# Kernel optimization log

Hardware: AMD Instinct MI355X
Metric: run time of the kernel (lower is better)

The kernel has to match this reference:

```python
import jax, jax.numpy as jnp
import numpy as np

QUERY_DIM = 512
KEY_DIM = 512
NUM_HEADS = 16
HEAD_DIM = QUERY_DIM // NUM_HEADS


def setup_inputs() -> dict:
    key = jax.random.key(0)
    ks = jax.random.split(key, 10)
    B, T, S = 4, 2048, 2048
    s_q = 1.0 / np.sqrt(QUERY_DIM)
    s_k = 1.0 / np.sqrt(KEY_DIM)
    return {
        "x": jax.random.normal(ks[0], (B, T, QUERY_DIM), dtype=jnp.float32),
        "context": jax.random.normal(ks[1], (B, S, KEY_DIM), dtype=jnp.float32),
        "Wq": jax.random.normal(ks[2], (QUERY_DIM, QUERY_DIM), dtype=jnp.float32) * s_q,
        "bq": jnp.zeros((QUERY_DIM,), dtype=jnp.float32),
        "Wk": jax.random.normal(ks[3], (KEY_DIM, QUERY_DIM), dtype=jnp.float32) * s_k,
        "bk": jnp.zeros((QUERY_DIM,), dtype=jnp.float32),
        "Wv": jax.random.normal(ks[4], (KEY_DIM, QUERY_DIM), dtype=jnp.float32) * s_k,
        "bv": jnp.zeros((QUERY_DIM,), dtype=jnp.float32),
        "Wo": jax.random.normal(ks[5], (QUERY_DIM, QUERY_DIM), dtype=jnp.float32) * s_q,
        "bo": jnp.zeros((QUERY_DIM,), dtype=jnp.float32),
    }


def reference(x, context, Wq, bq, Wk, bk, Wv, bv, Wo, bo):
    B, T, C = x.shape
    S = context.shape[1]
    H, D = NUM_HEADS, HEAD_DIM
    scale = D ** -0.5
    # projections -> [B, H, T/S, D]
    q = (x @ Wq + bq).reshape(B, T, H, D).transpose(0, 2, 1, 3)
    k = (context @ Wk + bk).reshape(B, S, H, D).transpose(0, 2, 1, 3)
    v = (context @ Wv + bv).reshape(B, S, H, D).transpose(0, 2, 1, 3)
    # explicit attention matrix [B, H, T, S] (faithful to the unfused original)
    attn = jnp.einsum("bhtd,bhsd->bhts", q, k) * scale
    attn = jax.nn.softmax(attn, axis=-1)  # dropout is identity in eval mode
    out = jnp.einsum("bhts,bhsd->bhtd", attn, v)
    out = out.transpose(0, 2, 1, 3).reshape(B, T, C)
    return out @ Wo + bo
```

## Files before the change

### kernel.cpp

```cpp
#include <hip/hip_runtime.h>
#include <hip/hip_bf16.h>
#include <cmath>

typedef __bf16 bf16;
typedef __bf16 bf16x2 __attribute__((ext_vector_type(2)));
typedef __bf16 bf16x4 __attribute__((ext_vector_type(4)));
typedef __bf16 bf16x8 __attribute__((ext_vector_type(8)));
typedef float floatx4 __attribute__((ext_vector_type(4)));
typedef unsigned int uintx2 __attribute__((ext_vector_type(2)));
typedef unsigned int uintx4 __attribute__((ext_vector_type(4)));

#define MFMA_BF16(a, b, c) __builtin_amdgcn_mfma_f32_16x16x32_bf16((a), (b), (c), 0, 0, 0)

#if defined(__has_builtin)
#if __has_builtin(__builtin_amdgcn_global_load_lds)
#define HAVE_GLL 1
#endif
#if __has_builtin(__builtin_amdgcn_cvt_pk_bf16_f32)
#define HAVE_PKCVT 1
#endif
#if __has_builtin(__builtin_amdgcn_permlane32_swap) && __has_builtin(__builtin_amdgcn_permlane16_swap)
#define HAVE_PLSWAP 1
#endif
#endif

__device__ __forceinline__ void stage16(const bf16* g, bf16* ldsbase, int lane) {
#ifdef HAVE_GLL
    __builtin_amdgcn_global_load_lds((const __attribute__((address_space(1))) unsigned int*)g,
                                     (__attribute__((address_space(3))) unsigned int*)ldsbase,
                                     16, 0, 0);
#else
    *(int4*)(ldsbase + lane * 8) = *(const int4*)g;
#endif
}

__device__ __forceinline__ unsigned pk2(float a, float b) {
    bf16x2 t;
#ifdef HAVE_PKCVT
    t = __builtin_amdgcn_cvt_pk_bf16_f32(a, b);
#else
    t[0] = (bf16)a;
    t[1] = (bf16)b;
#endif
    return __builtin_bit_cast(unsigned, t);
}

__device__ __forceinline__ uintx2 p32swap(unsigned x, unsigned y) {
#ifdef HAVE_PLSWAP
    auto r = __builtin_amdgcn_permlane32_swap(x, y, false, false);
    uintx2 o;
    o[0] = r[0];
    o[1] = r[1];
    return o;
#else
    const int lane = threadIdx.x & 63;
    const unsigned px = __shfl(x, lane ^ 32);
    const unsigned py = __shfl(y, lane ^ 32);
    uintx2 o;
    o[0] = (lane & 32) ? py : x;
    o[1] = (lane & 32) ? y : px;
    return o;
#endif
}

__device__ __forceinline__ uintx2 p16swap(unsigned x, unsigned y) {
#ifdef HAVE_PLSWAP
    auto r = __builtin_amdgcn_permlane16_swap(x, y, false, false);
    uintx2 o;
    o[0] = r[0];
    o[1] = r[1];
    return o;
#else
    const int lane = threadIdx.x & 63;
    const unsigned px = __shfl(x, lane ^ 16);
    const unsigned py = __shfl(y, lane ^ 16);
    uintx2 o;
    o[0] = (lane & 16) ? py : x;
    o[1] = (lane & 16) ? y : px;
    return o;
#endif
}

__device__ __forceinline__ int detect_bf16(const void* x) {
    const unsigned short* u = (const unsigned short*)x;
    const int lane = threadIdx.x & 63;
    const unsigned short w0 = u[4 * lane], w1 = u[4 * lane + 2];
    const int e0 = (w0 >> 7) & 0xFF, e1 = (w1 >> 7) & 0xFF;
    const unsigned long long b0 = __ballot(e0 >= 96 && e0 <= 158);
    const unsigned long long b1 = __ballot(e1 >= 96 && e1 <= 158);
    return (__popcll(b0) + __popcll(b1)) >= 90;
}

struct PrepArgs {
    const void* x;
    const void* ctx;
    const void* W[4];
    const void* bias[4];
    bf16* xc;
    bf16* ctxc;
    bf16* WT[4];
    bf16* biasc;
};

__global__ __launch_bounds__(256) void prep(PrepArgs a) {
    const int tid = threadIdx.x;
    const int f = detect_bf16(a.x);
    const int bid = blockIdx.x;
    if (bid < 1024) {
        const int w = bid >> 8, tileid = bid & 255;
        const int bx = tileid & 15, by = tileid >> 4;
        const void* __restrict__ in = a.W[w];
        bf16* __restrict__ out = a.WT[w];
        __shared__ bf16 tile[32][33];
        const int tx = tid & 31, ty = tid >> 5;
        const int x = bx * 32 + tx;
        const int y0 = by * 32;
#pragma unroll
        for (int yy = ty; yy < 32; yy += 8) {
            const size_t idx = (size_t)(y0 + yy) * 512 + x;
            const float v = f ? (float)((const bf16*)in)[idx] : ((const float*)in)[idx];
            tile[yy][tx] = (bf16)v;
        }
        __syncthreads();
        const int xo = by * 32 + tx;
        const int y1 = bx * 32;
#pragma unroll
        for (int yy = ty; yy < 32; yy += 8)
            out[(size_t)(y1 + yy) * 512 + xo] = tile[tx][yy];
    } else if (bid < 5120) {
        if (f) return;
        const int seg = (bid >= 3072);
        const void* src = seg ? a.ctx : a.x;
        bf16* dst = seg ? a.ctxc : a.xc;
        const int off = (bid - (seg ? 3072 : 1024)) * 256 + tid;
        const float4 p = ((const float4*)src)[2 * off];
        const float4 q = ((const float4*)src)[2 * off + 1];
        bf16x8 o;
        o[0] = (bf16)p.x; o[1] = (bf16)p.y; o[2] = (bf16)p.z; o[3] = (bf16)p.w;
        o[4] = (bf16)q.x; o[5] = (bf16)q.y; o[6] = (bf16)q.z; o[7] = (bf16)q.w;
        *(bf16x8*)(dst + (size_t)off * 8) = o;
    } else {
        for (int e = tid; e < 2048; e += 256) {
            const int seg = e >> 9, off = e & 511;
            const float v =
                f ? (float)((const bf16*)a.bias[seg])[off] : ((const float*)a.bias[seg])[off];
            a.biasc[seg * 512 + off] = (bf16)v;
        }
    }
}

struct QkvArgs {
    const void* xraw;
    const void* ctxraw;
    const bf16* Aconv[3];
    const bf16* Wt[3];
    const bf16* bias;
    bf16* out[3];
    float scale[3];
};

__global__ __launch_bounds__(256) void gemm_qkv(QkvArgs a) {
    __shared__ __align__(16) bf16 lA[2][128 * 32];
    __shared__ __align__(16) bf16 lB[2][128 * 32];
    const int z = blockIdx.z;
    const int f = detect_bf16(a.xraw);
    const bf16* __restrict__ A =
        f ? (const bf16*)(z == 0 ? a.xraw : a.ctxraw) : a.Aconv[z];
    const bf16* __restrict__ Wt = a.Wt[z];
    const int tid = threadIdx.x, wave = tid >> 6, lane = tid & 63;
    const int qd = lane >> 4, j = lane & 15;
    const int m0 = blockIdx.x * 128, n0 = blockIdx.y * 128;
    const int wrow = (wave & 1) * 64, wcol = (wave >> 1) * 64;
    const int srow = wave * 16 + (lane >> 2);
    const int scol = (lane & 3) * 8;
    const bf16* agp = A + (size_t)(m0 + srow) * 512 + scol;
    const bf16* bgp = Wt + (size_t)(n0 + srow) * 512 + scol;

    auto stage = [&](int buf, int k0) {
        stage16(agp + k0, &lA[buf][wave * 512], lane);
        stage16(agp + k0 + (size_t)64 * 512, &lA[buf][wave * 512 + 2048], lane);
        stage16(bgp + k0, &lB[buf][wave * 512], lane);
        stage16(bgp + k0 + (size_t)64 * 512, &lB[buf][wave * 512 + 2048], lane);
    };

    floatx4 acc[4][4] = {};

    stage(0, 0);
    int cur = 0;
#pragma unroll 1
    for (int it = 0; it < 16; ++it) {
        if (it < 15) {
            stage(cur ^ 1, (it + 1) * 32);
            asm volatile("s_waitcnt vmcnt(4)" ::: "memory");
        } else {
            asm volatile("s_waitcnt vmcnt(0)" ::: "memory");
        }
        __builtin_amdgcn_sched_barrier(0);
        __builtin_amdgcn_s_barrier();
        __builtin_amdgcn_sched_barrier(0);

        bf16x8 af[4], bfr[4];
#pragma unroll
        for (int i = 0; i < 4; ++i) {
            af[i] = *(const bf16x8*)(&lA[cur][(wrow + i * 16 + j) * 32 + qd * 8]);
            bfr[i] = *(const bf16x8*)(&lB[cur][(wcol + i * 16 + j) * 32 + qd * 8]);
        }
        if (z < 2) {
#pragma unroll
            for (int nt = 0; nt < 4; ++nt)
#pragma unroll
                for (int rf = 0; rf < 4; ++rf)
                    acc[nt][rf] = MFMA_BF16(bfr[nt], af[rf], acc[nt][rf]);
        } else {
#pragma unroll
            for (int rf = 0; rf < 4; ++rf)
#pragma unroll
                for (int nt = 0; nt < 4; ++nt)
                    acc[rf][nt] = MFMA_BF16(af[rf], bfr[nt], acc[rf][nt]);
        }

        __builtin_amdgcn_sched_barrier(0);
        __builtin_amdgcn_s_barrier();
        __builtin_amdgcn_sched_barrier(0);
        cur ^= 1;
    }

    const float scale = a.scale[z];
    const bf16* bias = a.bias + z * 512;
    bf16* __restrict__ C = a.out[z];
    if (z < 2) {
#pragma unroll
        for (int nt = 0; nt < 4; ++nt) {
            const int nb = n0 + wcol + nt * 16 + qd * 4;
            const bf16x4 bv4 = *(const bf16x4*)(bias + nb);
            const int h = nb >> 5, d0 = nb & 31;
#pragma unroll
            for (int rf = 0; rf < 4; ++rf) {
                const int m = m0 + wrow + rf * 16 + j;
                const int bb = m >> 11, t = m & 2047;
                bf16x4 pk;
#pragma unroll
                for (int r = 0; r < 4; ++r)
                    pk[r] = (bf16)((acc[nt][rf][r] + (float)bv4[r]) * scale);
                *(bf16x4*)(&C[(((size_t)bb * 16 + h) * 2048 + t) * 32 + d0]) = pk;
            }
        }
    } else {
#pragma unroll
        for (int nt = 0; nt < 4; ++nt) {
            const int n = n0 + wcol + nt * 16 + j;
            const float bv = (float)bias[n];
            const int h = n >> 5, d = n & 31;
#pragma unroll
            for (int rf = 0; rf < 4; ++rf) {
                const int t0 = m0 + wrow + rf * 16 + qd * 4;
                const int bb = t0 >> 11, s = t0 & 2047;
                bf16x4 pk;
#pragma unroll
                for (int r = 0; r < 4; ++r) pk[r] = (bf16)(acc[rf][nt][r] + bv);
                *(bf16x4*)(&C[(((size_t)bb * 16 + h) * 32 + d) * 2048 + s]) = pk;
            }
        }
    }
}

__device__ __forceinline__ void gll16kv(const bf16* g, bf16* lds) {
#ifdef HAVE_GLL
    __builtin_amdgcn_global_load_lds((const __attribute__((address_space(1))) unsigned int*)g,
                                     (__attribute__((address_space(3))) unsigned int*)lds,
                                     16, 0, 0);
#else
    *(int4*)(lds + (threadIdx.x & 63) * 8) = *(const int4*)g;
#endif
}

__global__ __launch_bounds__(256, 4) void attn_kernel(const bf16* __restrict__ Q,
                                                      const bf16* __restrict__ Kh,
                                                      const bf16* __restrict__ Vt,
                                                      bf16* __restrict__ O) {
    const int tid = threadIdx.x;
    const int wave = tid >> 6, lane = tid & 63;
    const int qd = lane >> 4, j = lane & 15;
    const int bh = blockIdx.x;
    const int b = bh >> 4, h = bh & 15;
    const int tw = blockIdx.y * 128 + wave * 32;

    __shared__ __align__(16) bf16 lsK[2][2][2048];
    __shared__ __align__(16) bf16 lsV[2][2][2048];

    const bf16* qbase = Q + ((size_t)bh * 2048 + tw) * 32;
    const bf16* kbase = Kh + (size_t)bh * 2048 * 32;
    const bf16* vbase = Vt + (size_t)bh * 32 * 2048;

    bf16x8 qf[2];
#pragma unroll
    for (int tf = 0; tf < 2; ++tf)
        qf[tf] = *(const bf16x8*)(qbase + (size_t)(tf * 16 + j) * 32 + qd * 8);

    const bf16* ksrc = kbase + (size_t)(wave * 16 + j) * 32 + qd * 8;
    const bf16* vsrc =
        vbase + (size_t)((wave >> 1) * 16 + j) * 2048 + (wave & 1) * 32 + qd * 8;
    bf16* kdst = &lsK[0][0][wave * 512];
    bf16* vdst = &lsV[0][0][wave * 512];

    auto stage = [&](int buf, int s0) {
        gll16kv(ksrc + (size_t)s0 * 32, kdst + buf * 4096);
        gll16kv(ksrc + (size_t)(s0 + 64) * 32, kdst + buf * 4096 + 2048);
        gll16kv(vsrc + s0, vdst + buf * 4096);
        gll16kv(vsrc + s0 + 64, vdst + buf * 4096 + 2048);
    };

    bf16x8 ones;
#pragma unroll
    for (int e = 0; e < 8; ++e) ones[e] = (bf16)1.0f;

    const floatx4 zero = {0.f, 0.f, 0.f, 0.f};
    floatx4 oacc[2][2] = {};
    floatx4 dacc[2] = {};

    auto qk = [&](const bf16* lk, bf16x8* pf) {
        bf16x8 kf[4];
#pragma unroll
        for (int sf = 0; sf < 4; ++sf)
            kf[sf] = *(const bf16x8*)(lk + sf * 512 + lane * 8);
#pragma unroll
        for (int tf = 0; tf < 2; ++tf) {
            floatx4 sc[4];
#pragma unroll
            for (int sf = 0; sf < 4; ++sf) sc[sf] = MFMA_BF16(kf[sf], qf[tf], zero);
            unsigned SW[4][2];
#pragma unroll
            for (int sf = 0; sf < 4; ++sf) {
                const float e0 = __builtin_amdgcn_exp2f(sc[sf][0]);
                const float e1 = __builtin_amdgcn_exp2f(sc[sf][1]);
                const float e2 = __builtin_amdgcn_exp2f(sc[sf][2]);
                const float e3 = __builtin_amdgcn_exp2f(sc[sf][3]);
                SW[sf][0] = pk2(e0, e1);
                SW[sf][1] = pk2(e2, e3);
            }
            const uintx2 a0 = p32swap(SW[0][0], SW[1][0]);
            const uintx2 a1 = p32swap(SW[0][1], SW[1][1]);
            const uintx2 c0 = p32swap(SW[2][0], SW[3][0]);
            const uintx2 c1 = p32swap(SW[2][1], SW[3][1]);
            const uintx2 t0 = p16swap(a0[0], a0[1]);
            const uintx2 t1 = p16swap(a1[0], a1[1]);
            const uintx2 t2 = p16swap(c0[0], c0[1]);
            const uintx2 t3 = p16swap(c1[0], c1[1]);
            uintx4 w0, w1;
            w0[0] = t0[0]; w0[1] = t1[0]; w0[2] = t0[1]; w0[3] = t1[1];
            w1[0] = t2[0]; w1[1] = t3[0]; w1[2] = t2[1]; w1[3] = t3[1];
            pf[tf * 2 + 0] = __builtin_bit_cast(bf16x8, w0);
            pf[tf * 2 + 1] = __builtin_bit_cast(bf16x8, w1);
        }
    };
    auto pv = [&](const bf16* lv, const bf16x8* pf) {
        bf16x8 vf[4];
#pragma unroll
        for (int i = 0; i < 4; ++i)
            vf[i] = *(const bf16x8*)(lv + i * 512 + lane * 8);
#pragma unroll
        for (int tf = 0; tf < 2; ++tf) {
            oacc[tf][0] = MFMA_BF16(pf[tf * 2 + 0], vf[0], oacc[tf][0]);
            oacc[tf][1] = MFMA_BF16(pf[tf * 2 + 0], vf[2], oacc[tf][1]);
            dacc[tf] = MFMA_BF16(pf[tf * 2 + 0], ones, dacc[tf]);
            oacc[tf][0] = MFMA_BF16(pf[tf * 2 + 1], vf[1], oacc[tf][0]);
            oacc[tf][1] = MFMA_BF16(pf[tf * 2 + 1], vf[3], oacc[tf][1]);
            dacc[tf] = MFMA_BF16(pf[tf * 2 + 1], ones, dacc[tf]);
        }
    };

    stage(0, 0);

    int cur = 0;
#pragma unroll 1
    for (int ph = 0; ph < 16; ++ph) {
        if (ph < 15) {
            stage(cur ^ 1, (ph + 1) * 128);
            asm volatile("s_waitcnt vmcnt(4)" ::: "memory");
        } else {
            asm volatile("s_waitcnt vmcnt(0)" ::: "memory");
        }
        __builtin_amdgcn_sched_barrier(0);
        __builtin_amdgcn_s_barrier();
        __builtin_amdgcn_sched_barrier(0);

        bf16x8 pfA[4], pfB[4];
        qk(&lsK[cur][0][0], pfA);
        qk(&lsK[cur][1][0], pfB);
        pv(&lsV[cur][0][0], pfA);
        pv(&lsV[cur][1][0], pfB);

        __builtin_amdgcn_sched_barrier(0);
        __builtin_amdgcn_s_barrier();
        __builtin_amdgcn_sched_barrier(0);
        cur ^= 1;
    }

#pragma unroll
    for (int tf = 0; tf < 2; ++tf)
#pragma unroll
        for (int r = 0; r < 4; ++r) {
            const float inv = 1.0f / dacc[tf][r];
            const int t = tw + tf * 16 + qd * 4 + r;
#pragma unroll
            for (int dt = 0; dt < 2; ++dt)
                O[((size_t)b * 2048 + t) * 512 + h * 32 + dt * 16 + j] =
                    (bf16)(oacc[tf][dt][r] * inv);
        }
}

__global__ __launch_bounds__(256) void gemm_out(const bf16* __restrict__ A,
                                                const bf16* __restrict__ Wt,
                                                const bf16* __restrict__ bias,
                                                void* __restrict__ C,
                                                const void* __restrict__ xraw) {
    __shared__ __align__(16) bf16 lA[2][128 * 32];
    __shared__ __align__(16) bf16 lB[2][128 * 32];
    const int oflag = detect_bf16(xraw);
    const int tid = threadIdx.x, wave = tid >> 6, lane = tid & 63;
    const int qd = lane >> 4, j = lane & 15;
    const int m0 = blockIdx.x * 128, n0 = blockIdx.y * 128;
    const int wrow = (wave & 1) * 64, wcol = (wave >> 1) * 64;
    const int srow = wave * 16 + (lane >> 2);
    const int scol = (lane & 3) * 8;
    const bf16* agp = A + (size_t)(m0 + srow) * 512 + scol;
    const bf16* bgp = Wt + (size_t)(n0 + srow) * 512 + scol;

    auto stage = [&](int buf, int k0) {
        stage16(agp + k0, &lA[buf][wave * 512], lane);
        stage16(agp + k0 + (size_t)64 * 512, &lA[buf][wave * 512 + 2048], lane);
        stage16(bgp + k0, &lB[buf][wave * 512], lane);
        stage16(bgp + k0 + (size_t)64 * 512, &lB[buf][wave * 512 + 2048], lane);
    };

    floatx4 acc[4][4] = {};

    stage(0, 0);
    int cur = 0;
#pragma unroll 1
    for (int it = 0; it < 16; ++it) {
        if (it < 15) {
            stage(cur ^ 1, (it + 1) * 32);
            asm volatile("s_waitcnt vmcnt(4)" ::: "memory");
        } else {
            asm volatile("s_waitcnt vmcnt(0)" ::: "memory");
        }
        __builtin_amdgcn_sched_barrier(0);
        __builtin_amdgcn_s_barrier();
        __builtin_amdgcn_sched_barrier(0);

        bf16x8 af[4], bfr[4];
#pragma unroll
        for (int i = 0; i < 4; ++i) {
            af[i] = *(const bf16x8*)(&lA[cur][(wrow + i * 16 + j) * 32 + qd * 8]);
            bfr[i] = *(const bf16x8*)(&lB[cur][(wcol + i * 16 + j) * 32 + qd * 8]);
        }
#pragma unroll
        for (int nt = 0; nt < 4; ++nt)
#pragma unroll
            for (int rf = 0; rf < 4; ++rf)
                acc[nt][rf] = MFMA_BF16(bfr[nt], af[rf], acc[nt][rf]);

        __builtin_amdgcn_sched_barrier(0);
        __builtin_amdgcn_s_barrier();
        __builtin_amdgcn_sched_barrier(0);
        cur ^= 1;
    }

#pragma unroll
    for (int nt = 0; nt < 4; ++nt) {
        const int nb = n0 + wcol + nt * 16 + qd * 4;
        const bf16x4 bv4 = *(const bf16x4*)(bias + nb);
#pragma unroll
        for (int rf = 0; rf < 4; ++rf) {
            const int m = m0 + wrow + rf * 16 + j;
            if (oflag) {
                bf16x4 pk;
#pragma unroll
                for (int r = 0; r < 4; ++r) pk[r] = (bf16)(acc[nt][rf][r] + (float)bv4[r]);
                *(bf16x4*)((bf16*)C + (size_t)m * 512 + nb) = pk;
            } else {
                float4 v;
                v.x = acc[nt][rf][0] + (float)bv4[0];
                v.y = acc[nt][rf][1] + (float)bv4[1];
                v.z = acc[nt][rf][2] + (float)bv4[2];
                v.w = acc[nt][rf][3] + (float)bv4[3];
                *(float4*)((float*)C + (size_t)m * 512 + nb) = v;
            }
        }
    }
}

extern "C" void kernel_launch(void* const* d_in, const int* in_sizes, int n_in, void* d_out,
                              int out_size, void* d_ws, size_t ws_size, hipStream_t stream) {
    char* ws = (char*)d_ws;
    bf16* wqT = (bf16*)(ws + 1048576);
    bf16* wkT = (bf16*)(ws + 1572864);
    bf16* wvT = (bf16*)(ws + 2097152);
    bf16* woT = (bf16*)(ws + 2621440);
    bf16* biasc = (bf16*)(ws + 3145728);
    bf16* xc = (bf16*)(ws + 4194304);
    bf16* ctxc = (bf16*)(ws + 12582912);
    bf16* qws = (bf16*)(ws + 20971520);
    bf16* kws = (bf16*)(ws + 29360128);
    bf16* vtws = (bf16*)(ws + 37748736);
    bf16* aws = xc;

    PrepArgs pa;
    pa.x = d_in[0]; pa.ctx = d_in[1];
    pa.W[0] = d_in[2]; pa.W[1] = d_in[4]; pa.W[2] = d_in[6]; pa.W[3] = d_in[8];
    pa.bias[0] = d_in[3]; pa.bias[1] = d_in[5]; pa.bias[2] = d_in[7]; pa.bias[3] = d_in[9];
    pa.xc = xc; pa.ctxc = ctxc;
    pa.WT[0] = wqT; pa.WT[1] = wkT; pa.WT[2] = wvT; pa.WT[3] = woT;
    pa.biasc = biasc;
    prep<<<5121, 256, 0, stream>>>(pa);

    QkvArgs qa;
    qa.xraw = d_in[0]; qa.ctxraw = d_in[1];
    qa.Aconv[0] = xc; qa.Aconv[1] = ctxc; qa.Aconv[2] = ctxc;
    qa.Wt[0] = wqT; qa.Wt[1] = wkT; qa.Wt[2] = wvT;
    qa.bias = biasc;
    qa.out[0] = qws; qa.out[1] = kws; qa.out[2] = vtws;
    qa.scale[0] = 0.2550348593f; qa.scale[1] = 1.0f; qa.scale[2] = 1.0f;
    gemm_qkv<<<dim3(64, 4, 3), 256, 0, stream>>>(qa);

    attn_kernel<<<dim3(64, 16), 256, 0, stream>>>(qws, kws, vtws, aws);

    gemm_out<<<dim3(64, 4), 256, 0, stream>>>(aws, woT, biasc + 3 * 512, d_out, d_in[0]);
}
```

Measured before the change: 197.6 us.

## Fuse fp32-to-bf16 conversion and weight transpose into GEMM loaders, drop prep kernel

Removes the separate prep kernel that converted x/context to bf16 and transposed and converted the weights. The QKV and output GEMMs now load raw fp32 (or bf16) activations and weights into registers, pack them to bf16, and write them into LDS with an in-register transpose for W. This saves one launch and a full round trip of converted x/context through global memory. In exchange, the GEMM main loops lose the async global-to-LDS path, wait for all loads each iteration, and do scalar 2-byte LDS stores for the B tile, which may cause bank conflicts.

After: 210.6 us. 6.6% more time.

```diff
diff --git a/kernel.cpp b/kernel.cpp
--- a/kernel.cpp
+++ b/kernel.cpp
@@ -7,6 +7,7 @@
 typedef __bf16 bf16x4 __attribute__((ext_vector_type(4)));
 typedef __bf16 bf16x8 __attribute__((ext_vector_type(8)));
 typedef float floatx4 __attribute__((ext_vector_type(4)));
+typedef int intx4 __attribute__((ext_vector_type(4)));
 typedef unsigned int uintx2 __attribute__((ext_vector_type(2)));
 typedef unsigned int uintx4 __attribute__((ext_vector_type(4)));
 
@@ -34,6 +35,22 @@
 #endif
 }
 
+__device__ __forceinline__ float4 gload16f(const float* p) {
+    float4 r;
+    asm volatile("global_load_dwordx4 %0, %1, off" : "=v"(r) : "v"(p));
+    return r;
+}
+__device__ __forceinline__ bf16x8 gload16h(const bf16* p) {
+    intx4 r;
+    asm volatile("global_load_dwordx4 %0, %1, off" : "=v"(r) : "v"(p));
+    return __builtin_bit_cast(bf16x8, r);
+}
+#define VMCNT0()                                         \
+    do {                                                 \
+        asm volatile("s_waitcnt vmcnt(0)" ::: "memory"); \
+        __builtin_amdgcn_sched_barrier(0);               \
+    } while (0)
+
 __device__ __forceinline__ unsigned pk2(float a, float b) {
     bf16x2 t;
 #ifdef HAVE_PKCVT
@@ -43,6 +60,15 @@
     t[1] = (bf16)b;
 #endif
     return __builtin_bit_cast(unsigned, t);
+}
+
+__device__ __forceinline__ bf16x8 pack8(const float4& a, const float4& b) {
+    uintx4 w;
+    w[0] = pk2(a.x, a.y);
+    w[1] = pk2(a.z, a.w);
+    w[2] = pk2(b.x, b.y);
+    w[3] = pk2(b.z, b.w);
+    return __builtin_bit_cast(bf16x8, w);
 }
 
 __device__ __forceinline__ uintx2 p32swap(unsigned x, unsigned y) {
@@ -62,7 +88,6 @@
     return o;
 #endif
 }
-
 __device__ __forceinline__ uintx2 p16swap(unsigned x, unsigned y) {
 #ifdef HAVE_PLSWAP
     auto r = __builtin_amdgcn_permlane16_swap(x, y, false, false);
@@ -91,119 +116,97 @@
     return (__popcll(b0) + __popcll(b1)) >= 90;
 }
 
-struct PrepArgs {
-    const void* x;
-    const void* ctx;
-    const void* W[4];
-    const void* bias[4];
-    bf16* xc;
-    bf16* ctxc;
-    bf16* WT[4];
-    bf16* biasc;
-};
-
-__global__ __launch_bounds__(256) void prep(PrepArgs a) {
-    const int tid = threadIdx.x;
-    const int f = detect_bf16(a.x);
-    const int bid = blockIdx.x;
-    if (bid < 1024) {
-        const int w = bid >> 8, tileid = bid & 255;
-        const int bx = tileid & 15, by = tileid >> 4;
-        const void* __restrict__ in = a.W[w];
-        bf16* __restrict__ out = a.WT[w];
-        __shared__ bf16 tile[32][33];
-        const int tx = tid & 31, ty = tid >> 5;
-        const int x = bx * 32 + tx;
-        const int y0 = by * 32;
-#pragma unroll
-        for (int yy = ty; yy < 32; yy += 8) {
-            const size_t idx = (size_t)(y0 + yy) * 512 + x;
-            const float v = f ? (float)((const bf16*)in)[idx] : ((const float*)in)[idx];
-            tile[yy][tx] = (bf16)v;
-        }
-        __syncthreads();
-        const int xo = by * 32 + tx;
-        const int y1 = bx * 32;
-#pragma unroll
-        for (int yy = ty; yy < 32; yy += 8)
-            out[(size_t)(y1 + yy) * 512 + xo] = tile[tx][yy];
-    } else if (bid < 5120) {
-        if (f) return;
-        const int seg = (bid >= 3072);
-        const void* src = seg ? a.ctx : a.x;
-        bf16* dst = seg ? a.ctxc : a.xc;
-        const int off = (bid - (seg ? 3072 : 1024)) * 256 + tid;
-        const float4 p = ((const float4*)src)[2 * off];
-        const float4 q = ((const float4*)src)[2 * off + 1];
-        bf16x8 o;
-        o[0] = (bf16)p.x; o[1] = (bf16)p.y; o[2] = (bf16)p.z; o[3] = (bf16)p.w;
-        o[4] = (bf16)q.x; o[5] = (bf16)q.y; o[6] = (bf16)q.z; o[7] = (bf16)q.w;
-        *(bf16x8*)(dst + (size_t)off * 8) = o;
-    } else {
-        for (int e = tid; e < 2048; e += 256) {
-            const int seg = e >> 9, off = e & 511;
-            const float v =
-                f ? (float)((const bf16*)a.bias[seg])[off] : ((const float*)a.bias[seg])[off];
-            a.biasc[seg * 512 + off] = (bf16)v;
-        }
-    }
-}
-
 struct QkvArgs {
     const void* xraw;
     const void* ctxraw;
-    const bf16* Aconv[3];
-    const bf16* Wt[3];
-    const bf16* bias;
+    const void* W[3];
+    const void* bias[3];
     bf16* out[3];
     float scale[3];
 };
 
 __global__ __launch_bounds__(256) void gemm_qkv(QkvArgs a) {
-    __shared__ __align__(16) bf16 lA[2][128 * 32];
-    __shared__ __align__(16) bf16 lB[2][128 * 32];
+    __shared__ __align__(16) bf16 lsA[2][4096];
+    __shared__ __align__(16) bf16 lsB[2][4096];
     const int z = blockIdx.z;
     const int f = detect_bf16(a.xraw);
-    const bf16* __restrict__ A =
-        f ? (const bf16*)(z == 0 ? a.xraw : a.ctxraw) : a.Aconv[z];
-    const bf16* __restrict__ Wt = a.Wt[z];
     const int tid = threadIdx.x, wave = tid >> 6, lane = tid & 63;
     const int qd = lane >> 4, j = lane & 15;
     const int m0 = blockIdx.x * 128, n0 = blockIdx.y * 128;
     const int wrow = (wave & 1) * 64, wcol = (wave >> 1) * 64;
-    const int srow = wave * 16 + (lane >> 2);
-    const int scol = (lane & 3) * 8;
-    const bf16* agp = A + (size_t)(m0 + srow) * 512 + scol;
-    const bf16* bgp = Wt + (size_t)(n0 + srow) * 512 + scol;
+
+    const void* Araw = (z == 0) ? a.xraw : a.ctxraw;
+    const void* Wraw = a.W[z];
+
+    const int srow = wave * 16 + (lane >> 2), scol = (lane & 3) * 8;
+    const bf16* agp = (const bf16*)Araw + (size_t)(m0 + srow) * 512 + scol;
+    const float* Af = (const float*)Araw;
+    const int am = m0 + wave * 32 + (lane >> 1), ah = (lane & 1) * 16;
+    const int bk = lane >> 1, bnl = (lane & 1) * 8;
+    const bf16* Wh = (const bf16*)Wraw;
+    const float* Wf = (const float*)Wraw;
+    const size_t bcol = (size_t)(n0 + wave * 32 + bnl);
+
+    float4 ar[4], br[4];
+    bf16x8 bh0, bh1;
 
     auto stage = [&](int buf, int k0) {
-        stage16(agp + k0, &lA[buf][wave * 512], lane);
-        stage16(agp + k0 + (size_t)64 * 512, &lA[buf][wave * 512 + 2048], lane);
-        stage16(bgp + k0, &lB[buf][wave * 512], lane);
-        stage16(bgp + k0 + (size_t)64 * 512, &lB[buf][wave * 512 + 2048], lane);
+        if (f) {
+            stage16(agp + k0, &lsA[buf][wave * 512], lane);
+            stage16(agp + k0 + (size_t)64 * 512, &lsA[buf][wave * 512 + 2048], lane);
+            const bf16* bp = Wh + (size_t)(k0 + bk) * 512 + bcol;
+            bh0 = gload16h(bp);
+            bh1 = gload16h(bp + 16);
+        } else {
+            const float* ap = Af + (size_t)am * 512 + k0 + ah;
+            ar[0] = gload16f(ap);
+            ar[1] = gload16f(ap + 4);
+            ar[2] = gload16f(ap + 8);
+            ar[3] = gload16f(ap + 12);
+            const float* bp = Wf + (size_t)(k0 + bk) * 512 + bcol;
+            br[0] = gload16f(bp);
+            br[1] = gload16f(bp + 4);
+            br[2] = gload16f(bp + 16);
+            br[3] = gload16f(bp + 20);
+        }
+    };
+    auto finish = [&](int buf) {
+        bf16x8 b0, b1;
+        if (f) {
+            b0 = bh0;
+            b1 = bh1;
+        } else {
+            b0 = pack8(br[0], br[1]);
+            b1 = pack8(br[2], br[3]);
+            bf16* ad = &lsA[buf][(wave * 32 + (lane >> 1)) * 32 + ah];
+            *(bf16x8*)ad = pack8(ar[0], ar[1]);
+            *(bf16x8*)(ad + 8) = pack8(ar[2], ar[3]);
+        }
+        const int nb0 = wave * 32 + bnl;
+#pragma unroll
+        for (int e = 0; e < 8; ++e) {
+            lsB[buf][(nb0 + e) * 32 + bk] = b0[e];
+            lsB[buf][(nb0 + 16 + e) * 32 + bk] = b1[e];
+        }
     };
 
     floatx4 acc[4][4] = {};
 
     stage(0, 0);
+    VMCNT0();
+    finish(0);
+    __syncthreads();
+
     int cur = 0;
 #pragma unroll 1
     for (int it = 0; it < 16; ++it) {
-        if (it < 15) {
-            stage(cur ^ 1, (it + 1) * 32);
-            asm volatile("s_waitcnt vmcnt(4)" ::: "memory");
-        } else {
-            asm volatile("s_waitcnt vmcnt(0)" ::: "memory");
-        }
-        __builtin_amdgcn_sched_barrier(0);
-        __builtin_amdgcn_s_barrier();
-        __builtin_amdgcn_sched_barrier(0);
+        if (it < 15) stage(cur ^ 1, (it + 1) * 32);
 
         bf16x8 af[4], bfr[4];
 #pragma unroll
         for (int i = 0; i < 4; ++i) {
-            af[i] = *(const bf16x8*)(&lA[cur][(wrow + i * 16 + j) * 32 + qd * 8]);
-            bfr[i] = *(const bf16x8*)(&lB[cur][(wcol + i * 16 + j) * 32 + qd * 8]);
+            af[i] = *(const bf16x8*)(&lsA[cur][(wrow + i * 16 + j) * 32 + qd * 8]);
+            bfr[i] = *(const bf16x8*)(&lsB[cur][(wcol + i * 16 + j) * 32 + qd * 8]);
         }
         if (z < 2) {
 #pragma unroll
@@ -219,46 +222,56 @@
                     acc[rf][nt] = MFMA_BF16(af[rf], bfr[nt], acc[rf][nt]);
         }
 
-        __builtin_amdgcn_sched_barrier(0);
-        __builtin_amdgcn_s_barrier();
-        __builtin_amdgcn_sched_barrier(0);
+        if (it < 15) {
+            VMCNT0();
+            finish(cur ^ 1);
+        }
+        __syncthreads();
         cur ^= 1;
     }
 
     const float scale = a.scale[z];
-    const bf16* bias = a.bias + z * 512;
     bf16* __restrict__ C = a.out[z];
     if (z < 2) {
 #pragma unroll
         for (int nt = 0; nt < 4; ++nt) {
             const int nb = n0 + wcol + nt * 16 + qd * 4;
-            const bf16x4 bv4 = *(const bf16x4*)(bias + nb);
+            float bvf[4];
+            if (f) {
+                const bf16x4 t = *(const bf16x4*)((const bf16*)a.bias[z] + nb);
+#pragma unroll
+                for (int r = 0; r < 4; ++r) bvf[r] = (float)t[r];
+            } else {
+                const float4 t = *(const float4*)((const float*)a.bias[z] + nb);
+                bvf[0] = t.x; bvf[1] = t.y; bvf[2] = t.z; bvf[3] = t.w;
+            }
             const int h = nb >> 5, d0 = nb & 31;
 #pragma unroll
             for (int rf = 0; rf < 4; ++rf) {
                 const int m = m0 + wrow + rf * 16 + j;
-                const int bb = m >> 11, t = m & 2047;
+                const int bb2 = m >> 11, t = m & 2047;
                 bf16x4 pk;
 #pragma unroll
                 for (int r = 0; r < 4; ++r)
-                    pk[r] = (bf16)((acc[nt][rf][r] + (float)bv4[r]) * scale);
-                *(bf16x4*)(&C[(((size_t)bb * 16 + h) * 2048 + t) * 32 + d0]) = pk;
+                    pk[r] = (bf16)((acc[nt][rf][r] + bvf[r]) * scale);
+                *(bf16x4*)(&C[(((size_t)bb2 * 16 + h) * 2048 + t) * 32 + d0]) = pk;
             }
         }
     } else {
 #pragma unroll
         for (int nt = 0; nt < 4; ++nt) {
             const int n = n0 + wcol + nt * 16 + j;
-            const float bv = (float)bias[n];
+            const float bv = f ? (float)((const bf16*)a.bias[z])[n]
+                               : ((const float*)a.bias[z])[n];
             const int h = n >> 5, d = n & 31;
 #pragma unroll
             for (int rf = 0; rf < 4; ++rf) {
                 const int t0 = m0 + wrow + rf * 16 + qd * 4;
-                const int bb = t0 >> 11, s = t0 & 2047;
+                const int bb2 = t0 >> 11, s = t0 & 2047;
                 bf16x4 pk;
 #pragma unroll
                 for (int r = 0; r < 4; ++r) pk[r] = (bf16)(acc[rf][nt][r] + bv);
-                *(bf16x4*)(&C[(((size_t)bb * 16 + h) * 32 + d) * 2048 + s]) = pk;
+                *(bf16x4*)(&C[(((size_t)bb2 * 16 + h) * 32 + d) * 2048 + s]) = pk;
             }
         }
     }
@@ -410,50 +423,76 @@
 }
 
 __global__ __launch_bounds__(256) void gemm_out(const bf16* __restrict__ A,
-                                                const bf16* __restrict__ Wt,
-                                                const bf16* __restrict__ bias,
+                                                const void* __restrict__ Wraw,
+                                                const void* __restrict__ biasraw,
                                                 void* __restrict__ C,
                                                 const void* __restrict__ xraw) {
-    __shared__ __align__(16) bf16 lA[2][128 * 32];
-    __shared__ __align__(16) bf16 lB[2][128 * 32];
-    const int oflag = detect_bf16(xraw);
+    __shared__ __align__(16) bf16 lsA[2][4096];
+    __shared__ __align__(16) bf16 lsB[2][4096];
+    const int f = detect_bf16(xraw);
     const int tid = threadIdx.x, wave = tid >> 6, lane = tid & 63;
     const int qd = lane >> 4, j = lane & 15;
     const int m0 = blockIdx.x * 128, n0 = blockIdx.y * 128;
     const int wrow = (wave & 1) * 64, wcol = (wave >> 1) * 64;
-    const int srow = wave * 16 + (lane >> 2);
-    const int scol = (lane & 3) * 8;
+    const int srow = wave * 16 + (lane >> 2), scol = (lane & 3) * 8;
     const bf16* agp = A + (size_t)(m0 + srow) * 512 + scol;
-    const bf16* bgp = Wt + (size_t)(n0 + srow) * 512 + scol;
+    const int bk = lane >> 1, bnl = (lane & 1) * 8;
+    const bf16* Wh = (const bf16*)Wraw;
+    const float* Wf = (const float*)Wraw;
+    const size_t bcol = (size_t)(n0 + wave * 32 + bnl);
+
+    float4 br[4];
+    bf16x8 bh0, bh1;
 
     auto stage = [&](int buf, int k0) {
-        stage16(agp + k0, &lA[buf][wave * 512], lane);
-        stage16(agp + k0 + (size_t)64 * 512, &lA[buf][wave * 512 + 2048], lane);
-        stage16(bgp + k0, &lB[buf][wave * 512], lane);
-        stage16(bgp + k0 + (size_t)64 * 512, &lB[buf][wave * 512 + 2048], lane);
+        stage16(agp + k0, &lsA[buf][wave * 512], lane);
+        stage16(agp + k0 + (size_t)64 * 512, &lsA[buf][wave * 512 + 2048], lane);
+        if (f) {
+            const bf16* bp = Wh + (size_t)(k0 + bk) * 512 + bcol;
+            bh0 = gload16h(bp);
+            bh1 = gload16h(bp + 16);
+        } else {
+            const float* bp = Wf + (size_t)(k0 + bk) * 512 + bcol;
+            br[0] = gload16f(bp);
+            br[1] = gload16f(bp + 4);
+            br[2] = gload16f(bp + 16);
+            br[3] = gload16f(bp + 20);
+        }
+    };
+    auto finish = [&](int buf) {
+        bf16x8 b0, b1;
+        if (f) {
+            b0 = bh0;
+            b1 = bh1;
+        } else {
+            b0 = pack8(br[0], br[1]);
+            b1 = pack8(br[2], br[3]);
+        }
+        const int nb0 = wave * 32 + bnl;
+#pragma unroll
+        for (int e = 0; e < 8; ++e) {
+            lsB[buf][(nb0 + e) * 32 + bk] = b0[e];
+            lsB[buf][(nb0 + 16 + e) * 32 + bk] = b1[e];
+        }
     };
 
     floatx4 acc[4][4] = {};
 
     stage(0, 0);
+    VMCNT0();
+    finish(0);
+    __syncthreads();
+
     int cur = 0;
 #pragma unroll 1
     for (int it = 0; it < 16; ++it) {
-        if (it < 15) {
-            stage(cur ^ 1, (it + 1) * 32);
-            asm volatile("s_waitcnt vmcnt(4)" ::: "memory");
-        } else {
-            asm volatile("s_waitcnt vmcnt(0)" ::: "memory");
-        }
-        __builtin_amdgcn_sched_barrier(0);
-        __builtin_amdgcn_s_barrier();
-        __builtin_amdgcn_sched_barrier(0);
+        if (it < 15) stage(cur ^ 1, (it + 1) * 32);
 
         bf16x8 af[4], bfr[4];
 #pragma unroll
         for (int i = 0; i < 4; ++i) {
-            af[i] = *(const bf16x8*)(&lA[cur][(wrow + i * 16 + j) * 32 + qd * 8]);
-            bfr[i] = *(const bf16x8*)(&lB[cur][(wcol + i * 16 + j) * 32 + qd * 8]);
+            af[i] = *(const bf16x8*)(&lsA[cur][(wrow + i * 16 + j) * 32 + qd * 8]);
+            bfr[i] = *(const bf16x8*)(&lsB[cur][(wcol + i * 16 + j) * 32 + qd * 8]);
         }
 #pragma unroll
         for (int nt = 0; nt < 4; ++nt)
@@ -461,30 +500,40 @@
             for (int rf = 0; rf < 4; ++rf)
                 acc[nt][rf] = MFMA_BF16(bfr[nt], af[rf], acc[nt][rf]);
 
-        __builtin_amdgcn_sched_barrier(0);
-        __builtin_amdgcn_s_barrier();
-        __builtin_amdgcn_sched_barrier(0);
+        if (it < 15) {
+            VMCNT0();
+            finish(cur ^ 1);
+        }
+        __syncthreads();
         cur ^= 1;
     }
 
 #pragma unroll
     for (int nt = 0; nt < 4; ++nt) {
         const int nb = n0 + wcol + nt * 16 + qd * 4;
-        const bf16x4 bv4 = *(const bf16x4*)(bias + nb);
+        float bvf[4];
+        if (f) {
+            const bf16x4 t = *(const bf16x4*)((const bf16*)biasraw + nb);
+#pragma unroll
+            for (int r = 0; r < 4; ++r) bvf[r] = (float)t[r];
+        } else {
+            const float4 t = *(const float4*)((const float*)biasraw + nb);
+            bvf[0] = t.x; bvf[1] = t.y; bvf[2] = t.z; bvf[3] = t.w;
+        }
 #pragma unroll
         for (int rf = 0; rf < 4; ++rf) {
             const int m = m0 + wrow + rf * 16 + j;
-            if (oflag) {
+            if (f) {
                 bf16x4 pk;
 #pragma unroll
-                for (int r = 0; r < 4; ++r) pk[r] = (bf16)(acc[nt][rf][r] + (float)bv4[r]);
+                for (int r = 0; r < 4; ++r) pk[r] = (bf16)(acc[nt][rf][r] + bvf[r]);
                 *(bf16x4*)((bf16*)C + (size_t)m * 512 + nb) = pk;
             } else {
                 float4 v;
-                v.x = acc[nt][rf][0] + (float)bv4[0];
-                v.y = acc[nt][rf][1] + (float)bv4[1];
-                v.z = acc[nt][rf][2] + (float)bv4[2];
-                v.w = acc[nt][rf][3] + (float)bv4[3];
+                v.x = acc[nt][rf][0] + bvf[0];
+                v.y = acc[nt][rf][1] + bvf[1];
+                v.z = acc[nt][rf][2] + bvf[2];
+                v.w = acc[nt][rf][3] + bvf[3];
                 *(float4*)((float*)C + (size_t)m * 512 + nb) = v;
             }
         }
@@ -494,37 +543,20 @@
 extern "C" void kernel_launch(void* const* d_in, const int* in_sizes, int n_in, void* d_out,
                               int out_size, void* d_ws, size_t ws_size, hipStream_t stream) {
     char* ws = (char*)d_ws;
-    bf16* wqT = (bf16*)(ws + 1048576);
-    bf16* wkT = (bf16*)(ws + 1572864);
-    bf16* wvT = (bf16*)(ws + 2097152);
-    bf16* woT = (bf16*)(ws + 2621440);
-    bf16* biasc = (bf16*)(ws + 3145728);
-    bf16* xc = (bf16*)(ws + 4194304);
-    bf16* ctxc = (bf16*)(ws + 12582912);
+    bf16* aws = (bf16*)(ws + 4194304);
     bf16* qws = (bf16*)(ws + 20971520);
     bf16* kws = (bf16*)(ws + 29360128);
     bf16* vtws = (bf16*)(ws + 37748736);
-    bf16* aws = xc;
-
-    PrepArgs pa;
-    pa.x = d_in[0]; pa.ctx = d_in[1];
-    pa.W[0] = d_in[2]; pa.W[1] = d_in[4]; pa.W[2] = d_in[6]; pa.W[3] = d_in[8];
-    pa.bias[0] = d_in[3]; pa.bias[1] = d_in[5]; pa.bias[2] = d_in[7]; pa.bias[3] = d_in[9];
-    pa.xc = xc; pa.ctxc = ctxc;
-    pa.WT[0] = wqT; pa.WT[1] = wkT; pa.WT[2] = wvT; pa.WT[3] = woT;
-    pa.biasc = biasc;
-    prep<<<5121, 256, 0, stream>>>(pa);
 
     QkvArgs qa;
     qa.xraw = d_in[0]; qa.ctxraw = d_in[1];
-    qa.Aconv[0] = xc; qa.Aconv[1] = ctxc; qa.Aconv[2] = ctxc;
-    qa.Wt[0] = wqT; qa.Wt[1] = wkT; qa.Wt[2] = wvT;
-    qa.bias = biasc;
+    qa.W[0] = d_in[2]; qa.W[1] = d_in[4]; qa.W[2] = d_in[6];
+    qa.bias[0] = d_in[3]; qa.bias[1] = d_in[5]; qa.bias[2] = d_in[7];
     qa.out[0] = qws; qa.out[1] = kws; qa.out[2] = vtws;
     qa.scale[0] = 0.2550348593f; qa.scale[1] = 1.0f; qa.scale[2] = 1.0f;
     gemm_qkv<<<dim3(64, 4, 3), 256, 0, stream>>>(qa);
 
     attn_kernel<<<dim3(64, 16), 256, 0, stream>>>(qws, kws, vtws, aws);
 
-    gemm_out<<<dim3(64, 4), 256, 0, stream>>>(aws, woT, biasc + 3 * 512, d_out, d_in[0]);
-}
+    gemm_out<<<dim3(64, 4), 256, 0, stream>>>(aws, d_in[8], d_in[9], d_out, d_in[0]);
+}
```

## Fuse fp32-to-bf16 activation conversion into QKV GEMM A-operand staging

Applied to the files above, without the earlier changes.

Drops the separate conversion of x and context to bf16 from the prep kernel. The QKV GEMM now loads fp32 activations straight into registers, packs them to bf16, and writes them to a padded LDS tile while the next B tile streams in asynchronously. Biases are read raw in the epilogues instead of from a pre-converted buffer. This removes a full-activation write and re-read pass to global memory, but each QKV GEMM block now reads fp32 A (double the bytes), and K and V blocks each convert the context separately, in a loop that waits on all loads before every LDS write.

Measured after the change: 195.1 us. No clear change (-1.2%).

```diff
diff --git a/kernel.cpp b/kernel.cpp
--- a/kernel.cpp
+++ b/kernel.cpp
@@ -7,6 +7,7 @@
 typedef __bf16 bf16x4 __attribute__((ext_vector_type(4)));
 typedef __bf16 bf16x8 __attribute__((ext_vector_type(8)));
 typedef float floatx4 __attribute__((ext_vector_type(4)));
+typedef int intx4 __attribute__((ext_vector_type(4)));
 typedef unsigned int uintx2 __attribute__((ext_vector_type(2)));
 typedef unsigned int uintx4 __attribute__((ext_vector_type(4)));
 
@@ -34,6 +35,17 @@
 #endif
 }
 
+__device__ __forceinline__ float4 gload16f(const float* p) {
+    float4 r;
+    asm volatile("global_load_dwordx4 %0, %1, off" : "=v"(r) : "v"(p));
+    return r;
+}
+#define VMCNT0()                                         \
+    do {                                                 \
+        asm volatile("s_waitcnt vmcnt(0)" ::: "memory"); \
+        __builtin_amdgcn_sched_barrier(0);               \
+    } while (0)
+
 __device__ __forceinline__ unsigned pk2(float a, float b) {
     bf16x2 t;
 #ifdef HAVE_PKCVT
@@ -43,6 +55,15 @@
     t[1] = (bf16)b;
 #endif
     return __builtin_bit_cast(unsigned, t);
+}
+
+__device__ __forceinline__ bf16x8 pack8(const float4& a, const float4& b) {
+    uintx4 w;
+    w[0] = pk2(a.x, a.y);
+    w[1] = pk2(a.z, a.w);
+    w[2] = pk2(b.x, b.y);
+    w[3] = pk2(b.z, b.w);
+    return __builtin_bit_cast(bf16x8, w);
 }
 
 __device__ __forceinline__ uintx2 p32swap(unsigned x, unsigned y) {
@@ -62,7 +83,6 @@
     return o;
 #endif
 }
-
 __device__ __forceinline__ uintx2 p16swap(unsigned x, unsigned y) {
 #ifdef HAVE_PLSWAP
     auto r = __builtin_amdgcn_permlane16_swap(x, y, false, false);
@@ -91,119 +111,99 @@
     return (__popcll(b0) + __popcll(b1)) >= 90;
 }
 
-struct PrepArgs {
+struct PrepWArgs {
     const void* x;
-    const void* ctx;
     const void* W[4];
-    const void* bias[4];
-    bf16* xc;
-    bf16* ctxc;
     bf16* WT[4];
-    bf16* biasc;
 };
 
-__global__ __launch_bounds__(256) void prep(PrepArgs a) {
+__global__ __launch_bounds__(256) void prep_w(PrepWArgs a) {
     const int tid = threadIdx.x;
     const int f = detect_bf16(a.x);
     const int bid = blockIdx.x;
-    if (bid < 1024) {
-        const int w = bid >> 8, tileid = bid & 255;
-        const int bx = tileid & 15, by = tileid >> 4;
-        const void* __restrict__ in = a.W[w];
-        bf16* __restrict__ out = a.WT[w];
-        __shared__ bf16 tile[32][33];
-        const int tx = tid & 31, ty = tid >> 5;
-        const int x = bx * 32 + tx;
-        const int y0 = by * 32;
-#pragma unroll
-        for (int yy = ty; yy < 32; yy += 8) {
-            const size_t idx = (size_t)(y0 + yy) * 512 + x;
-            const float v = f ? (float)((const bf16*)in)[idx] : ((const float*)in)[idx];
-            tile[yy][tx] = (bf16)v;
-        }
-        __syncthreads();
-        const int xo = by * 32 + tx;
-        const int y1 = bx * 32;
-#pragma unroll
-        for (int yy = ty; yy < 32; yy += 8)
-            out[(size_t)(y1 + yy) * 512 + xo] = tile[tx][yy];
-    } else if (bid < 5120) {
-        if (f) return;
-        const int seg = (bid >= 3072);
-        const void* src = seg ? a.ctx : a.x;
-        bf16* dst = seg ? a.ctxc : a.xc;
-        const int off = (bid - (seg ? 3072 : 1024)) * 256 + tid;
-        const float4 p = ((const float4*)src)[2 * off];
-        const float4 q = ((const float4*)src)[2 * off + 1];
-        bf16x8 o;
-        o[0] = (bf16)p.x; o[1] = (bf16)p.y; o[2] = (bf16)p.z; o[3] = (bf16)p.w;
-        o[4] = (bf16)q.x; o[5] = (bf16)q.y; o[6] = (bf16)q.z; o[7] = (bf16)q.w;
-        *(bf16x8*)(dst + (size_t)off * 8) = o;
-    } else {
-        for (int e = tid; e < 2048; e += 256) {
-            const int seg = e >> 9, off = e & 511;
-            const float v =
-                f ? (float)((const bf16*)a.bias[seg])[off] : ((const float*)a.bias[seg])[off];
-            a.biasc[seg * 512 + off] = (bf16)v;
-        }
+    const int w = bid >> 8, tileid = bid & 255;
+    const int bx = tileid & 15, by = tileid >> 4;
+    const void* __restrict__ in = a.W[w];
+    bf16* __restrict__ out = a.WT[w];
+    __shared__ bf16 tile[32][33];
+    const int tx = tid & 31, ty = tid >> 5;
+    const int x = bx * 32 + tx;
+    const int y0 = by * 32;
+#pragma unroll
+    for (int yy = ty; yy < 32; yy += 8) {
+        const size_t idx = (size_t)(y0 + yy) * 512 + x;
+        const float v = f ? (float)((const bf16*)in)[idx] : ((const float*)in)[idx];
+        tile[yy][tx] = (bf16)v;
     }
+    __syncthreads();
+    const int xo = by * 32 + tx;
+    const int y1 = bx * 32;
+#pragma unroll
+    for (int yy = ty; yy < 32; yy += 8)
+        out[(size_t)(y1 + yy) * 512 + xo] = tile[tx][yy];
 }
 
 struct QkvArgs {
     const void* xraw;
     const void* ctxraw;
-    const bf16* Aconv[3];
     const bf16* Wt[3];
-    const bf16* bias;
+    const void* bias[3];
     bf16* out[3];
     float scale[3];
 };
 
 __global__ __launch_bounds__(256) void gemm_qkv(QkvArgs a) {
-    __shared__ __align__(16) bf16 lA[2][128 * 32];
-    __shared__ __align__(16) bf16 lB[2][128 * 32];
+    __shared__ __align__(16) bf16 lsA[2][128 * 40];
+    __shared__ __align__(16) bf16 lsB[2][4096];
     const int z = blockIdx.z;
     const int f = detect_bf16(a.xraw);
-    const bf16* __restrict__ A =
-        f ? (const bf16*)(z == 0 ? a.xraw : a.ctxraw) : a.Aconv[z];
-    const bf16* __restrict__ Wt = a.Wt[z];
     const int tid = threadIdx.x, wave = tid >> 6, lane = tid & 63;
     const int qd = lane >> 4, j = lane & 15;
     const int m0 = blockIdx.x * 128, n0 = blockIdx.y * 128;
     const int wrow = (wave & 1) * 64, wcol = (wave >> 1) * 64;
-    const int srow = wave * 16 + (lane >> 2);
-    const int scol = (lane & 3) * 8;
-    const bf16* agp = A + (size_t)(m0 + srow) * 512 + scol;
+
+    const void* Araw = (z == 0) ? a.xraw : a.ctxraw;
+    const bf16* __restrict__ Wt = a.Wt[z];
+
+    const int srow = wave * 16 + (lane >> 2), scol = (lane & 3) * 8;
+    const bf16* agp = (const bf16*)Araw + (size_t)(m0 + srow) * 512 + scol;
     const bf16* bgp = Wt + (size_t)(n0 + srow) * 512 + scol;
-
-    auto stage = [&](int buf, int k0) {
-        stage16(agp + k0, &lA[buf][wave * 512], lane);
-        stage16(agp + k0 + (size_t)64 * 512, &lA[buf][wave * 512 + 2048], lane);
-        stage16(bgp + k0, &lB[buf][wave * 512], lane);
-        stage16(bgp + k0 + (size_t)64 * 512, &lB[buf][wave * 512 + 2048], lane);
+    const float* Af = (const float*)Araw;
+    const int arow = wave * 32 + (lane >> 1);
+    const int ah = (lane & 1) * 16;
+
+    const int SA = f ? 32 : 40;
+
+    float4 ar[4];
+    auto stageB = [&](int buf, int k0) {
+        stage16(bgp + k0, &lsB[buf][wave * 512], lane);
+        stage16(bgp + k0 + (size_t)64 * 512, &lsB[buf][wave * 512 + 2048], lane);
+    };
+    auto loadA = [&](int k0) {
+        const float* ap = Af + (size_t)(m0 + arow) * 512 + k0 + ah;
+        ar[0] = gload16f(ap);
+        ar[1] = gload16f(ap + 4);
+        ar[2] = gload16f(ap + 8);
+        ar[3] = gload16f(ap + 12);
+    };
+    auto writeA = [&](int buf) {
+        bf16* ad = &lsA[buf][arow * 40 + ah];
+        *(bf16x8*)ad = pack8(ar[0], ar[1]);
+        *(bf16x8*)(ad + 8) = pack8(ar[2], ar[3]);
+    };
+    auto stageA1 = [&](int buf, int k0) {
+        stage16(agp + k0, &lsA[buf][wave * 512], lane);
+        stage16(agp + k0 + (size_t)64 * 512, &lsA[buf][wave * 512 + 2048], lane);
     };
 
     floatx4 acc[4][4] = {};
 
-    stage(0, 0);
-    int cur = 0;
-#pragma unroll 1
-    for (int it = 0; it < 16; ++it) {
-        if (it < 15) {
-            stage(cur ^ 1, (it + 1) * 32);
-            asm volatile("s_waitcnt vmcnt(4)" ::: "memory");
-        } else {
-            asm volatile("s_waitcnt vmcnt(0)" ::: "memory");
-        }
-        __builtin_amdgcn_sched_barrier(0);
-        __builtin_amdgcn_s_barrier();
-        __builtin_amdgcn_sched_barrier(0);
-
+    auto compute = [&](int cur) {
         bf16x8 af[4], bfr[4];
 #pragma unroll
         for (int i = 0; i < 4; ++i) {
-            af[i] = *(const bf16x8*)(&lA[cur][(wrow + i * 16 + j) * 32 + qd * 8]);
-            bfr[i] = *(const bf16x8*)(&lB[cur][(wcol + i * 16 + j) * 32 + qd * 8]);
+            af[i] = *(const bf16x8*)(&lsA[cur][(wrow + i * 16 + j) * SA + qd * 8]);
+            bfr[i] = *(const bf16x8*)(&lsB[cur][(wcol + i * 16 + j) * 32 + qd * 8]);
         }
         if (z < 2) {
 #pragma unroll
@@ -218,47 +218,95 @@
                 for (int nt = 0; nt < 4; ++nt)
                     acc[rf][nt] = MFMA_BF16(af[rf], bfr[nt], acc[rf][nt]);
         }
-
-        __builtin_amdgcn_sched_barrier(0);
-        __builtin_amdgcn_s_barrier();
-        __builtin_amdgcn_sched_barrier(0);
-        cur ^= 1;
+    };
+
+    if (f) {
+        stageA1(0, 0);
+        stageB(0, 0);
+        int cur = 0;
+#pragma unroll 1
+        for (int it = 0; it < 16; ++it) {
+            if (it < 15) {
+                stageA1(cur ^ 1, (it + 1) * 32);
+                stageB(cur ^ 1, (it + 1) * 32);
+                asm volatile("s_waitcnt vmcnt(4)" ::: "memory");
+            } else {
+                asm volatile("s_waitcnt vmcnt(0)" ::: "memory");
+            }
+            __builtin_amdgcn_sched_barrier(0);
+            __builtin_amdgcn_s_barrier();
+            __builtin_amdgcn_sched_barrier(0);
+            compute(cur);
+            __builtin_amdgcn_sched_barrier(0);
+            __builtin_amdgcn_s_barrier();
+            __builtin_amdgcn_sched_barrier(0);
+            cur ^= 1;
+        }
+    } else {
+        stageB(0, 0);
+        loadA(0);
+        VMCNT0();
+        writeA(0);
+        __syncthreads();
+        int cur = 0;
+#pragma unroll 1
+        for (int it = 0; it < 16; ++it) {
+            if (it < 15) {
+                stageB(cur ^ 1, (it + 1) * 32);
+                loadA((it + 1) * 32);
+            }
+            compute(cur);
+            if (it < 15) {
+                VMCNT0();
+                writeA(cur ^ 1);
+            }
+            __syncthreads();
+            cur ^= 1;
+        }
     }
 
     const float scale = a.scale[z];
-    const bf16* bias = a.bias + z * 512;
     bf16* __restrict__ C = a.out[z];
     if (z < 2) {
 #pragma unroll
         for (int nt = 0; nt < 4; ++nt) {
             const int nb = n0 + wcol + nt * 16 + qd * 4;
-            const bf16x4 bv4 = *(const bf16x4*)(bias + nb);
+            float bvf[4];
+            if (f) {
+                const bf16x4 t = *(const bf16x4*)((const bf16*)a.bias[z] + nb);
+#pragma unroll
+                for (int r = 0; r < 4; ++r) bvf[r] = (float)t[r];
+            } else {
+                const float4 t = *(const float4*)((const float*)a.bias[z] + nb);
+                bvf[0] = t.x; bvf[1] = t.y; bvf[2] = t.z; bvf[3] = t.w;
+            }
             const int h = nb >> 5, d0 = nb & 31;
 #pragma unroll
             for (int rf = 0; rf < 4; ++rf) {
                 const int m = m0 + wrow + rf * 16 + j;
-                const int bb = m >> 11, t = m & 2047;
+                const int bb2 = m >> 11, t = m & 2047;
                 bf16x4 pk;
 #pragma unroll
                 for (int r = 0; r < 4; ++r)
-                    pk[r] = (bf16)((acc[nt][rf][r] + (float)bv4[r]) * scale);
-                *(bf16x4*)(&C[(((size_t)bb * 16 + h) * 2048 + t) * 32 + d0]) = pk;
+                    pk[r] = (bf16)((acc[nt][rf][r] + bvf[r]) * scale);
+                *(bf16x4*)(&C[(((size_t)bb2 * 16 + h) * 2048 + t) * 32 + d0]) = pk;
             }
         }
     } else {
 #pragma unroll
         for (int nt = 0; nt < 4; ++nt) {
             const int n = n0 + wcol + nt * 16 + j;
-            const float bv = (float)bias[n];
+            const float bv = f ? (float)((const bf16*)a.bias[z])[n]
+                               : ((const float*)a.bias[z])[n];
             const int h = n >> 5, d = n & 31;
 #pragma unroll
             for (int rf = 0; rf < 4; ++rf) {
                 const int t0 = m0 + wrow + rf * 16 + qd * 4;
-                const int bb = t0 >> 11, s = t0 & 2047;
+                const int bb2 = t0 >> 11, s = t0 & 2047;
                 bf16x4 pk;
 #pragma unroll
                 for (int r = 0; r < 4; ++r) pk[r] = (bf16)(acc[rf][nt][r] + bv);
-                *(bf16x4*)(&C[(((size_t)bb * 16 + h) * 32 + d) * 2048 + s]) = pk;
+                *(bf16x4*)(&C[(((size_t)bb2 * 16 + h) * 32 + d) * 2048 + s]) = pk;
             }
         }
     }
@@ -411,7 +459,7 @@
 
 __global__ __launch_bounds__(256) void gemm_out(const bf16* __restrict__ A,
                                                 const bf16* __restrict__ Wt,
-                                                const bf16* __restrict__ bias,
+                                                const void* __restrict__ biasraw,
                                                 void* __restrict__ C,
                                                 const void* __restrict__ xraw) {
     __shared__ __align__(16) bf16 lA[2][128 * 32];
@@ -470,21 +518,29 @@
 #pragma unroll
     for (int nt = 0; nt < 4; ++nt) {
         const int nb = n0 + wcol + nt * 16 + qd * 4;
-        const bf16x4 bv4 = *(const bf16x4*)(bias + nb);
+        float bvf[4];
+        if (oflag) {
+            const bf16x4 t = *(const bf16x4*)((const bf16*)biasraw + nb);
+#pragma unroll
+            for (int r = 0; r < 4; ++r) bvf[r] = (float)t[r];
+        } else {
+            const float4 t = *(const float4*)((const float*)biasraw + nb);
+            bvf[0] = t.x; bvf[1] = t.y; bvf[2] = t.z; bvf[3] = t.w;
+        }
 #pragma unroll
         for (int rf = 0; rf < 4; ++rf) {
             const int m = m0 + wrow + rf * 16 + j;
             if (oflag) {
                 bf16x4 pk;
 #pragma unroll
-                for (int r = 0; r < 4; ++r) pk[r] = (bf16)(acc[nt][rf][r] + (float)bv4[r]);
+                for (int r = 0; r < 4; ++r) pk[r] = (bf16)(acc[nt][rf][r] + bvf[r]);
                 *(bf16x4*)((bf16*)C + (size_t)m * 512 + nb) = pk;
             } else {
                 float4 v;
-                v.x = acc[nt][rf][0] + (float)bv4[0];
-                v.y = acc[nt][rf][1] + (float)bv4[1];
-                v.z = acc[nt][rf][2] + (float)bv4[2];
-                v.w = acc[nt][rf][3] + (float)bv4[3];
+                v.x = acc[nt][rf][0] + bvf[0];
+                v.y = acc[nt][rf][1] + bvf[1];
+                v.z = acc[nt][rf][2] + bvf[2];
+                v.w = acc[nt][rf][3] + bvf[3];
                 *(float4*)((float*)C + (size_t)m * 512 + nb) = v;
             }
         }
@@ -498,33 +554,26 @@
     bf16* wkT = (bf16*)(ws + 1572864);
     bf16* wvT = (bf16*)(ws + 2097152);
     bf16* woT = (bf16*)(ws + 2621440);
-    bf16* biasc = (bf16*)(ws + 3145728);
-    bf16* xc = (bf16*)(ws + 4194304);
-    bf16* ctxc = (bf16*)(ws + 12582912);
+    bf16* aws = (bf16*)(ws + 4194304);
     bf16* qws = (bf16*)(ws + 20971520);
     bf16* kws = (bf16*)(ws + 29360128);
     bf16* vtws = (bf16*)(ws + 37748736);
-    bf16* aws = xc;
-
-    PrepArgs pa;
-    pa.x = d_in[0]; pa.ctx = d_in[1];
-    pa.W[0] = d_in[2]; pa.W[1] = d_in[4]; pa.W[2] = d_in[6]; pa.W[3] = d_in[8];
-    pa.bias[0] = d_in[3]; pa.bias[1] = d_in[5]; pa.bias[2] = d_in[7]; pa.bias[3] = d_in[9];
-    pa.xc = xc; pa.ctxc = ctxc;
-    pa.WT[0] = wqT; pa.WT[1] = wkT; pa.WT[2] = wvT; pa.WT[3] = woT;
-    pa.biasc = biasc;
-    prep<<<5121, 256, 0, stream>>>(pa);
+
+    PrepWArgs pw;
+    pw.x = d_in[0];
+    pw.W[0] = d_in[2]; pw.W[1] = d_in[4]; pw.W[2] = d_in[6]; pw.W[3] = d_in[8];
+    pw.WT[0] = wqT; pw.WT[1] = wkT; pw.WT[2] = wvT; pw.WT[3] = woT;
+    prep_w<<<1024, 256, 0, stream>>>(pw);
 
     QkvArgs qa;
     qa.xraw = d_in[0]; qa.ctxraw = d_in[1];
-    qa.Aconv[0] = xc; qa.Aconv[1] = ctxc; qa.Aconv[2] = ctxc;
     qa.Wt[0] = wqT; qa.Wt[1] = wkT; qa.Wt[2] = wvT;
-    qa.bias = biasc;
+    qa.bias[0] = d_in[3]; qa.bias[1] = d_in[5]; qa.bias[2] = d_in[7];
     qa.out[0] = qws; qa.out[1] = kws; qa.out[2] = vtws;
     qa.scale[0] = 0.2550348593f; qa.scale[1] = 1.0f; qa.scale[2] = 1.0f;
     gemm_qkv<<<dim3(64, 4, 3), 256, 0, stream>>>(qa);
 
     attn_kernel<<<dim3(64, 16), 256, 0, stream>>>(qws, kws, vtws, aws);
 
-    gemm_out<<<dim3(64, 4), 256, 0, stream>>>(aws, woT, biasc + 3 * 512, d_out, d_in[0]);
-}
+    gemm_out<<<dim3(64, 4), 256, 0, stream>>>(aws, woT, d_in[9], d_out, d_in[0]);
+}
```
